# Performance work log

Measured on AMD Instinct MI355X. Metric: run time of the kernel, lower is better.

The kernel has to match this reference:

```python
import jax, jax.numpy as jnp
import numpy as np

N = 50000   # num_embs = num nodes
E = 800000  # num edges
D = 256     # feature dim
L = 4       # num layers
EPS = 1e-5


def setup_inputs() -> dict:
    key = jax.random.key(0)
    ks = jax.random.split(key, 8)
    scale = 1.0 / np.sqrt(D)
    return {
        "x": jax.random.normal(ks[0], (N, D), dtype=jnp.float32),  # ignored by forward
        "edge_index": jax.random.randint(ks[1], (2, E), 0, N, dtype=jnp.int32),
        "edge_weight": jax.random.uniform(ks[2], (E,), dtype=jnp.float32),
        "emb_weight": jax.random.normal(ks[3], (N, D), dtype=jnp.float32),
        "ln_w": jnp.ones((L, D), dtype=jnp.float32),
        "ln_b": jnp.zeros((L, D), dtype=jnp.float32),
        "conv_w": jax.random.normal(ks[4], (L, D, D), dtype=jnp.float32) * scale,
        "conv_b": jnp.zeros((L, D), dtype=jnp.float32),
        "post_w": jax.random.normal(ks[5], (D, D), dtype=jnp.float32) * scale,
        "post_b": jnp.zeros((D,), dtype=jnp.float32),
    }


def _layer_norm(h, w, b):
    mu = jnp.mean(h, axis=-1, keepdims=True)
    var = jnp.mean(jnp.square(h - mu), axis=-1, keepdims=True)
    return (h - mu) * jax.lax.rsqrt(var + EPS) * w + b


def reference(x, edge_index, edge_weight, emb_weight, ln_w, ln_b, conv_w, conv_b, post_w, post_b):
    # GCNConv semantics (PyG defaults): add self-loops (weight 1), symmetric norm.
    loop = jnp.arange(N, dtype=edge_index.dtype)
    src = jnp.concatenate([edge_index[0], loop])
    dst = jnp.concatenate([edge_index[1], loop])
    w = jnp.concatenate([edge_weight, jnp.ones((N,), edge_weight.dtype)])
    deg = jax.ops.segment_sum(w, dst, num_segments=N)
    dinv = jnp.where(deg > 0, jax.lax.rsqrt(jnp.maximum(deg, 1e-12)), 0.0)
    coef = (dinv[src] * w * dinv[dst])[:, None]  # [E+N, 1]

    h = emb_weight  # forward ignores x; cond_emb is None
    for i in range(L):
        z = _layer_norm(h, ln_w[i], ln_b[i])          # node LayerNorm
        zw = z @ conv_w[i]                             # linear transform
        agg = jax.ops.segment_sum(coef * zw[src], dst, num_segments=N)
        z = agg + conv_b[i]
        z = jax.nn.gelu(z, approximate=False)          # torch GELU is exact
        h = z + h                                      # residual (dropout=0)
    return h @ post_w + post_b
```

## Files before the change

kernel.cpp:

```cpp
#include <hip/hip_runtime.h>
#include <hip/hip_bf16.h>

#define N_NODES 50000
#define N_EDGES 800000
#define DIM     256
#define NLAYERS 4
#define EPS     1e-5f
#define SCAN_B  196
#define MASK40  ((1ULL << 40) - 1)
#define EPACK_CAP (N_EDGES + 15 * N_NODES + 32)
#define STRIDE  260

typedef __bf16 bf16x8 __attribute__((ext_vector_type(8)));
typedef float  f32x4  __attribute__((ext_vector_type(4)));
typedef float  f32x2  __attribute__((ext_vector_type(2)));
typedef unsigned short u16x8 __attribute__((ext_vector_type(8)));
typedef unsigned short u16x4 __attribute__((ext_vector_type(4)));
typedef int            i32x4 __attribute__((ext_vector_type(4)));
typedef unsigned int   u32x2 __attribute__((ext_vector_type(2)));

__device__ __forceinline__ unsigned short f2b(float f) {
    __hip_bfloat16 h = __float2bfloat16(f);
    return __builtin_bit_cast(unsigned short, h);
}
__device__ __forceinline__ float b2f(unsigned short u) {
    unsigned int v = ((unsigned int)u) << 16;
    return __builtin_bit_cast(float, v);
}
__device__ __forceinline__ float gelu_exact(float x) {
    return 0.5f * x * (1.0f + erff(x * 0.70710678118654752f));
}
__device__ __forceinline__ unsigned int pack_fp8x4(float a, float b, float c, float d) {
    int v = 0;
    v = __builtin_amdgcn_cvt_pk_fp8_f32(a, b, v, false);
    v = __builtin_amdgcn_cvt_pk_fp8_f32(c, d, v, true);
    return (unsigned int)v;
}

__global__ __launch_bounds__(256) void hist_kernel(const int* __restrict__ dst,
                                                   const float* __restrict__ w,
                                                   unsigned long long* __restrict__ cnt64,
                                                   int* __restrict__ rank) {
    int e = blockIdx.x * 256 + threadIdx.x;
    if (e >= N_EDGES) return;
    int d = dst[e];
    unsigned long long wfix = (unsigned long long)(w[e] * 4294967296.0f);
    unsigned long long old = atomicAdd(&cnt64[d], (1ULL << 40) | wfix);
    rank[e] = (int)(old >> 40);
}

__global__ __launch_bounds__(256) void scan_a_kernel(const unsigned long long* __restrict__ cnt64,
                                                     float* __restrict__ dinv,
                                                     int* __restrict__ bsum) {
    __shared__ int l[256];
    int i = blockIdx.x * 256 + threadIdx.x;
    int pc = 0;
    if (i < N_NODES) {
        unsigned long long v = cnt64[i];
        int cnt = (int)(v >> 40);
        float sw = (float)(v & MASK40) * 2.3283064365386963e-10f;
        dinv[i] = rsqrtf(1.0f + sw);
        pc = (cnt + 15) & ~15;
    }
    l[threadIdx.x] = pc;
    __syncthreads();
    for (int o = 128; o > 0; o >>= 1) {
        if (threadIdx.x < o) l[threadIdx.x] += l[threadIdx.x + o];
        __syncthreads();
    }
    if (threadIdx.x == 0) bsum[blockIdx.x] = l[0];
}

__global__ __launch_bounds__(256) void scan_b_kernel(const int* __restrict__ bsum,
                                                     int* __restrict__ boff,
                                                     int* __restrict__ rowptr) {
    __shared__ int l[256];
    int t = threadIdx.x;
    l[t] = (t < SCAN_B) ? bsum[t] : 0;
    __syncthreads();
    if (t == 0) {
        int run = 0;
        for (int j = 0; j < SCAN_B; ++j) { int v = l[j]; l[j] = run; run += v; }
        rowptr[N_NODES] = run;
    }
    __syncthreads();
    boff[t] = l[t];
}

__global__ __launch_bounds__(256) void scan_c_kernel(const unsigned long long* __restrict__ cnt64,
                                                     const int* __restrict__ boff,
                                                     int* __restrict__ rowptr) {
    __shared__ int l[256];
    int i = blockIdx.x * 256 + threadIdx.x;
    int pc = 0;
    if (i < N_NODES) {
        int cnt = (int)(cnt64[i] >> 40);
        pc = (cnt + 15) & ~15;
    }
    l[threadIdx.x] = pc;
    __syncthreads();
    if (threadIdx.x == 0) {
        int run = 0;
        for (int j = 0; j < 256; ++j) { int v = l[j]; l[j] = run; run += v; }
    }
    __syncthreads();
    if (i < N_NODES) rowptr[i] = boff[blockIdx.x] + l[threadIdx.x];
}

__global__ __launch_bounds__(256) void fill_kernel(const int* __restrict__ src,
                                                   const int* __restrict__ dst,
                                                   const float* __restrict__ w,
                                                   const float* __restrict__ dinv,
                                                   const int* __restrict__ rowptr,
                                                   const int* __restrict__ rank,
                                                   int2* __restrict__ epack) {
    int e = blockIdx.x * 256 + threadIdx.x;
    if (e >= N_EDGES) return;
    int s = src[e], d = dst[e];
    float c = dinv[s] * w[e] * dinv[d];
    int p = rowptr[d] + rank[e];
    epack[p] = make_int2(s << 8, __float_as_int(c));
}

__global__ __launch_bounds__(256) void convw_kernel(const float* __restrict__ conv_w,
                                                    const float* __restrict__ post_w,
                                                    unsigned short* __restrict__ Wt) {
    int idx = blockIdx.x * 256 + threadIdx.x;
    if (idx >= 5 * 65536) return;
    int m = idx >> 16;
    int r = idx & 65535;
    int n = r >> 8;
    int k = r & 255;
    float v = (m < 4) ? conv_w[m * 65536 + k * 256 + n] : post_w[k * 256 + n];
    Wt[idx] = f2b(v);
}

__global__ __launch_bounds__(256) void ln_cast_kernel(const float* __restrict__ H,
                                                      const float* __restrict__ lnw,
                                                      const float* __restrict__ lnb,
                                                      unsigned char* __restrict__ Z8,
                                                      unsigned short* __restrict__ Hbf) {
    int row = blockIdx.x * 4 + (threadIdx.x >> 6);
    int lane = threadIdx.x & 63;
    const float4 x = *(const float4*)(H + (size_t)row * DIM + lane * 4);
    float s = x.x + x.y + x.z + x.w;
    for (int o = 32; o > 0; o >>= 1) s += __shfl_xor(s, o);
    float mu = s * (1.0f / DIM);
    float d0 = x.x - mu, d1 = x.y - mu, d2 = x.z - mu, d3 = x.w - mu;
    float v = d0 * d0 + d1 * d1 + d2 * d2 + d3 * d3;
    for (int o = 32; o > 0; o >>= 1) v += __shfl_xor(v, o);
    float rs = rsqrtf(v * (1.0f / DIM) + EPS);
    const float4 ww = *(const float4*)(lnw + lane * 4);
    const float4 bb = *(const float4*)(lnb + lane * 4);
    float z0 = d0 * rs * ww.x + bb.x;
    float z1 = d1 * rs * ww.y + bb.y;
    float z2 = d2 * rs * ww.z + bb.z;
    float z3 = d3 * rs * ww.w + bb.w;
    *(unsigned int*)(Z8 + (size_t)row * DIM + lane * 4) = pack_fp8x4(z0, z1, z2, z3);
    ushort4 h4;
    h4.x = f2b(x.x); h4.y = f2b(x.y); h4.z = f2b(x.z); h4.w = f2b(x.w);
    *(ushort4*)(Hbf + (size_t)row * DIM + lane * 4) = h4;
}

__global__ __launch_bounds__(256) void agg_kernel(const unsigned char* __restrict__ Z8,
                                                  const int* __restrict__ rowptr,
                                                  const int2* __restrict__ epack,
                                                  const float* __restrict__ dinv,
                                                  unsigned short* __restrict__ AGG) {
    int node = blockIdx.x * 4 + (threadIdx.x >> 6);
    int lane = threadIdx.x & 63;
    int g = lane >> 5;
    int colB = (lane & 31) * 8;

    float di = dinv[node];
    float scg = (g == 0) ? di * di : 0.0f;
    const u32x2 zs = *(const u32x2*)(Z8 + (size_t)node * DIM + colB);
    f32x2 a0, a1, a2, a3;
    {
        f32x2 p0 = __builtin_amdgcn_cvt_pk_f32_fp8(zs[0], false);
        f32x2 p1 = __builtin_amdgcn_cvt_pk_f32_fp8(zs[0], true);
        f32x2 p2 = __builtin_amdgcn_cvt_pk_f32_fp8(zs[1], false);
        f32x2 p3 = __builtin_amdgcn_cvt_pk_f32_fp8(zs[1], true);
        a0 = scg * p0; a1 = scg * p1; a2 = scg * p2; a3 = scg * p3;
    }

    int e0 = rowptr[node], e1 = rowptr[node + 1];
    for (int e = e0; e < e1; e += 16) {
        const int2* pp = epack + e + 8 * g;
        const i32x4 q0 = *(const i32x4*)pp;
        const i32x4 q1 = *(const i32x4*)(pp + 2);
        const i32x4 q2 = *(const i32x4*)(pp + 4);
        const i32x4 q3 = *(const i32x4*)(pp + 6);
        const u32x2 v0 = *(const u32x2*)(Z8 + q0[0] + colB);
        const u32x2 v1 = *(const u32x2*)(Z8 + q0[2] + colB);
        const u32x2 v2 = *(const u32x2*)(Z8 + q1[0] + colB);
        const u32x2 v3 = *(const u32x2*)(Z8 + q1[2] + colB);
        const u32x2 v4 = *(const u32x2*)(Z8 + q2[0] + colB);
        const u32x2 v5 = *(const u32x2*)(Z8 + q2[2] + colB);
        const u32x2 v6 = *(const u32x2*)(Z8 + q3[0] + colB);
        const u32x2 v7 = *(const u32x2*)(Z8 + q3[2] + colB);
        float c0 = __int_as_float(q0[1]), c1 = __int_as_float(q0[3]);
        float c2 = __int_as_float(q1[1]), c3 = __int_as_float(q1[3]);
        float c4 = __int_as_float(q2[1]), c5 = __int_as_float(q2[3]);
        float c6 = __int_as_float(q3[1]), c7 = __int_as_float(q3[3]);
        #pragma unroll
        for (int h = 0; h < 8; ++h) {
            u32x2 vv; float cc;
            switch (h) {
                case 0: vv = v0; cc = c0; break;
                case 1: vv = v1; cc = c1; break;
                case 2: vv = v2; cc = c2; break;
                case 3: vv = v3; cc = c3; break;
                case 4: vv = v4; cc = c4; break;
                case 5: vv = v5; cc = c5; break;
                case 6: vv = v6; cc = c6; break;
                default: vv = v7; cc = c7; break;
            }
            f32x2 p0 = __builtin_amdgcn_cvt_pk_f32_fp8(vv[0], false);
            f32x2 p1 = __builtin_amdgcn_cvt_pk_f32_fp8(vv[0], true);
            f32x2 p2 = __builtin_amdgcn_cvt_pk_f32_fp8(vv[1], false);
            f32x2 p3 = __builtin_amdgcn_cvt_pk_f32_fp8(vv[1], true);
            a0 += cc * p0; a1 += cc * p1; a2 += cc * p2; a3 += cc * p3;
        }
    }
    float a[8] = {a0[0], a0[1], a1[0], a1[1], a2[0], a2[1], a3[0], a3[1]};
    #pragma unroll
    for (int j = 0; j < 8; ++j) a[j] += __shfl_xor(a[j], 32);

    if (g == 0) {
        u16x8 z;
        #pragma unroll
        for (int j = 0; j < 8; ++j) z[j] = f2b(a[j]);
        *(u16x8*)(AGG + (size_t)node * DIM + colB) = z;
    }
}

__global__ __launch_bounds__(256, 4) void gemm_fused_kernel(const unsigned short* __restrict__ A,
                                                            const unsigned short* __restrict__ Bt,
                                                            const float* __restrict__ bias,
                                                            unsigned short* __restrict__ Hbf,
                                                            const float* __restrict__ lnw,
                                                            const float* __restrict__ lnb,
                                                            unsigned char* __restrict__ Z8,
                                                            int doLN) {
    __shared__ unsigned short stile[32 * STRIDE];
    int tid = threadIdx.x;
    int wave = tid >> 6;
    int lane = tid & 63;
    int q = lane >> 4;
    int c16 = lane & 15;
    int mbase = blockIdx.x * 32;
    int cbase = wave * 64;

    const unsigned short* aptr[2];
    #pragma unroll
    for (int nt = 0; nt < 2; ++nt) {
        int row = mbase + nt * 16 + c16;
        if (row >= N_NODES) row = N_NODES - 1;
        aptr[nt] = A + (size_t)row * DIM + q * 8;
    }
    const unsigned short* wptr[4];
    #pragma unroll
    for (int ct = 0; ct < 4; ++ct)
        wptr[ct] = Bt + (size_t)(cbase + ct * 16 + c16) * DIM + q * 8;

    f32x4 acc[2][4] = {};
    bf16x8 nfc[2], wfc[4];
    #pragma unroll
    for (int nt = 0; nt < 2; ++nt)
        nfc[nt] = __builtin_bit_cast(bf16x8, *(const u16x8*)(aptr[nt]));
    #pragma unroll
    for (int ct = 0; ct < 4; ++ct)
        wfc[ct] = __builtin_bit_cast(bf16x8, *(const u16x8*)(wptr[ct]));

    #pragma unroll 1
    for (int k0 = 32; k0 < DIM; k0 += 32) {
        bf16x8 nfn[2], wfn[4];
        #pragma unroll
        for (int nt = 0; nt < 2; ++nt)
            nfn[nt] = __builtin_bit_cast(bf16x8, *(const u16x8*)(aptr[nt] + k0));
        #pragma unroll
        for (int ct = 0; ct < 4; ++ct)
            wfn[ct] = __builtin_bit_cast(bf16x8, *(const u16x8*)(wptr[ct] + k0));
        #pragma unroll
        for (int nt = 0; nt < 2; ++nt)
            #pragma unroll
            for (int ct = 0; ct < 4; ++ct)
                acc[nt][ct] = __builtin_amdgcn_mfma_f32_16x16x32_bf16(wfc[ct], nfc[nt], acc[nt][ct], 0, 0, 0);
        #pragma unroll
        for (int nt = 0; nt < 2; ++nt) nfc[nt] = nfn[nt];
        #pragma unroll
        for (int ct = 0; ct < 4; ++ct) wfc[ct] = wfn[ct];
    }
    #pragma unroll
    for (int nt = 0; nt < 2; ++nt)
        #pragma unroll
        for (int ct = 0; ct < 4; ++ct)
            acc[nt][ct] = __builtin_amdgcn_mfma_f32_16x16x32_bf16(wfc[ct], nfc[nt], acc[nt][ct], 0, 0, 0);

    #pragma unroll
    for (int nt = 0; nt < 2; ++nt) {
        int row = nt * 16 + c16;
        #pragma unroll
        for (int ct = 0; ct < 4; ++ct) {
            int col = cbase + ct * 16 + q * 4;
            u16x4 pk;
            pk[0] = f2b(acc[nt][ct][0]);
            pk[1] = f2b(acc[nt][ct][1]);
            pk[2] = f2b(acc[nt][ct][2]);
            pk[3] = f2b(acc[nt][ct][3]);
            *(u16x4*)&stile[row * STRIDE + col] = pk;
        }
    }
    __syncthreads();

    int r  = tid >> 3;
    int cb = (tid & 7) * 32;
    int node = mbase + r;
    if (node < N_NODES) {
        float h[32];
        float psum = 0.0f, psq = 0.0f;
        #pragma unroll
        for (int i = 0; i < 4; ++i) {
            const u16x8 sv = *(const u16x8*)&stile[r * STRIDE + cb + i * 8];
            const f32x4 b0 = *(const f32x4*)(bias + cb + i * 8);
            const f32x4 b1 = *(const f32x4*)(bias + cb + i * 8 + 4);
            const u16x8 hv = *(const u16x8*)(Hbf + (size_t)node * DIM + cb + i * 8);
            #pragma unroll
            for (int j = 0; j < 8; ++j) {
                float v = b2f(sv[j]) + (j < 4 ? b0[j] : b1[j - 4]);
                float hn = gelu_exact(v) + b2f(hv[j]);
                h[i * 8 + j] = hn;
                psum += hn;
                psq += hn * hn;
            }
        }
        #pragma unroll
        for (int i = 0; i < 4; ++i) {
            u16x8 hw;
            #pragma unroll
            for (int j = 0; j < 8; ++j) hw[j] = f2b(h[i * 8 + j]);
            *(u16x8*)(Hbf + (size_t)node * DIM + cb + i * 8) = hw;
        }
        if (doLN) {
            psum += __shfl_xor(psum, 1);
            psum += __shfl_xor(psum, 2);
            psum += __shfl_xor(psum, 4);
            psq  += __shfl_xor(psq, 1);
            psq  += __shfl_xor(psq, 2);
            psq  += __shfl_xor(psq, 4);
            float mu = psum * (1.0f / DIM);
            float var = fmaxf(psq * (1.0f / DIM) - mu * mu, 0.0f);
            float rs = rsqrtf(var + EPS);
            #pragma unroll
            for (int i2 = 0; i2 < 2; ++i2) {
                int c0 = cb + i2 * 16;
                unsigned int pk[4];
                #pragma unroll
                for (int k = 0; k < 4; ++k) {
                    const f32x4 ww = *(const f32x4*)(lnw + c0 + k * 4);
                    const f32x4 lb = *(const f32x4*)(lnb + c0 + k * 4);
                    int hb = i2 * 16 + k * 4;
                    float y0 = (h[hb + 0] - mu) * rs * ww[0] + lb[0];
                    float y1 = (h[hb + 1] - mu) * rs * ww[1] + lb[1];
                    float y2 = (h[hb + 2] - mu) * rs * ww[2] + lb[2];
                    float y3 = (h[hb + 3] - mu) * rs * ww[3] + lb[3];
                    pk[k] = pack_fp8x4(y0, y1, y2, y3);
                }
                uint4 st = make_uint4(pk[0], pk[1], pk[2], pk[3]);
                *(uint4*)(Z8 + (size_t)node * DIM + c0) = st;
            }
        }
    }
}

__global__ __launch_bounds__(256, 4) void gemm_out_kernel(const unsigned short* __restrict__ A,
                                                          const unsigned short* __restrict__ Bt,
                                                          float* __restrict__ C,
                                                          const float* __restrict__ bias) {
    int tid = threadIdx.x;
    int wave = tid >> 6;
    int lane = tid & 63;
    int q = lane >> 4;
    int c16 = lane & 15;
    int mbase = blockIdx.x * 32;
    int cbase = wave * 64;

    const unsigned short* aptr[2];
    #pragma unroll
    for (int nt = 0; nt < 2; ++nt) {
        int row = mbase + nt * 16 + c16;
        if (row >= N_NODES) row = N_NODES - 1;
        aptr[nt] = A + (size_t)row * DIM + q * 8;
    }
    const unsigned short* wptr[4];
    #pragma unroll
    for (int ct = 0; ct < 4; ++ct)
        wptr[ct] = Bt + (size_t)(cbase + ct * 16 + c16) * DIM + q * 8;

    f32x4 acc[2][4] = {};
    bf16x8 nfc[2], wfc[4];
    #pragma unroll
    for (int nt = 0; nt < 2; ++nt)
        nfc[nt] = __builtin_bit_cast(bf16x8, *(const u16x8*)(aptr[nt]));
    #pragma unroll
    for (int ct = 0; ct < 4; ++ct)
        wfc[ct] = __builtin_bit_cast(bf16x8, *(const u16x8*)(wptr[ct]));

    #pragma unroll 1
    for (int k0 = 32; k0 < DIM; k0 += 32) {
        bf16x8 nfn[2], wfn[4];
        #pragma unroll
        for (int nt = 0; nt < 2; ++nt)
            nfn[nt] = __builtin_bit_cast(bf16x8, *(const u16x8*)(aptr[nt] + k0));
        #pragma unroll
        for (int ct = 0; ct < 4; ++ct)
            wfn[ct] = __builtin_bit_cast(bf16x8, *(const u16x8*)(wptr[ct] + k0));
        #pragma unroll
        for (int nt = 0; nt < 2; ++nt)
            #pragma unroll
            for (int ct = 0; ct < 4; ++ct)
                acc[nt][ct] = __builtin_amdgcn_mfma_f32_16x16x32_bf16(nfc[nt], wfc[ct], acc[nt][ct], 0, 0, 0);
        #pragma unroll
        for (int nt = 0; nt < 2; ++nt) nfc[nt] = nfn[nt];
        #pragma unroll
        for (int ct = 0; ct < 4; ++ct) wfc[ct] = wfn[ct];
    }
    #pragma unroll
    for (int nt = 0; nt < 2; ++nt)
        #pragma unroll
        for (int ct = 0; ct < 4; ++ct)
            acc[nt][ct] = __builtin_amdgcn_mfma_f32_16x16x32_bf16(nfc[nt], wfc[ct], acc[nt][ct], 0, 0, 0);

    float bb[4];
    #pragma unroll
    for (int ct = 0; ct < 4; ++ct)
        bb[ct] = bias[cbase + ct * 16 + c16];
    #pragma unroll
    for (int nt = 0; nt < 2; ++nt) {
        #pragma unroll
        for (int j = 0; j < 4; ++j) {
            int node = mbase + nt * 16 + q * 4 + j;
            if (node >= N_NODES) continue;
            #pragma unroll
            for (int ct = 0; ct < 4; ++ct) {
                int chan = cbase + ct * 16 + c16;
                C[(size_t)node * DIM + chan] = acc[nt][ct][j] + bb[ct];
            }
        }
    }
}

extern "C" void kernel_launch(void* const* d_in, const int* in_sizes, int n_in,
                              void* d_out, int out_size, void* d_ws, size_t ws_size,
                              hipStream_t stream) {
    const int*   ei     = (const int*)d_in[1];
    const int*   src    = ei;
    const int*   dst    = ei + N_EDGES;
    const float* ew     = (const float*)d_in[2];
    const float* emb    = (const float*)d_in[3];
    const float* ln_w   = (const float*)d_in[4];
    const float* ln_b   = (const float*)d_in[5];
    const float* conv_w = (const float*)d_in[6];
    const float* conv_b = (const float*)d_in[7];
    const float* post_w = (const float*)d_in[8];
    const float* post_b = (const float*)d_in[9];
    float* out = (float*)d_out;

    char* w = (char*)d_ws;
    size_t off = 0;
    auto alloc = [&](size_t bytes) -> char* {
        char* p = w + off;
        off += (bytes + 255) & ~(size_t)255;
        return p;
    };
    unsigned long long* cnt64 = (unsigned long long*)alloc((size_t)N_NODES * 8);
    float* dinv   = (float*)alloc((size_t)N_NODES * 4);
    int*   rank   = (int*)alloc((size_t)N_EDGES * 4);
    int*   rowptr = (int*)alloc((size_t)(N_NODES + 1) * 4);
    int*   bsum   = (int*)alloc(256 * 4);
    int*   boff   = (int*)alloc(256 * 4);
    int2*  epack  = (int2*)alloc((size_t)EPACK_CAP * 8);
    unsigned short* Wt    = (unsigned short*)alloc((size_t)5 * 65536 * 2);
    unsigned short* AGG16 = (unsigned short*)alloc((size_t)N_NODES * DIM * 2);
    unsigned char*  Z8    = (unsigned char*)alloc((size_t)N_NODES * DIM);
    unsigned short* Hbf   = (unsigned short*)alloc((size_t)N_NODES * DIM * 2);

    hipMemsetAsync(cnt64, 0, (size_t)N_NODES * 8, stream);
    hipMemsetAsync(epack, 0, (size_t)EPACK_CAP * 8, stream);
    hist_kernel<<<N_EDGES / 256, 256, 0, stream>>>(dst, ew, cnt64, rank);
    scan_a_kernel<<<SCAN_B, 256, 0, stream>>>(cnt64, dinv, bsum);
    scan_b_kernel<<<1, 256, 0, stream>>>(bsum, boff, rowptr);
    scan_c_kernel<<<SCAN_B, 256, 0, stream>>>(cnt64, boff, rowptr);
    fill_kernel<<<N_EDGES / 256, 256, 0, stream>>>(src, dst, ew, dinv, rowptr, rank, epack);
    convw_kernel<<<(5 * 65536) / 256, 256, 0, stream>>>(conv_w, post_w, Wt);

    const int GEMM_GRID = (N_NODES + 31) / 32;
    ln_cast_kernel<<<N_NODES / 4, 256, 0, stream>>>(emb, ln_w, ln_b, Z8, Hbf);
    for (int l = 0; l < NLAYERS; ++l) {
        agg_kernel<<<N_NODES / 4, 256, 0, stream>>>(Z8, rowptr, epack, dinv, AGG16);
        int doLN = (l < NLAYERS - 1) ? 1 : 0;
        const float* nlw = doLN ? (ln_w + (l + 1) * DIM) : ln_w;
        const float* nlb = doLN ? (ln_b + (l + 1) * DIM) : ln_b;
        gemm_fused_kernel<<<GEMM_GRID, 256, 0, stream>>>(AGG16, Wt + (size_t)l * 65536,
                                                         conv_b + (size_t)l * DIM, Hbf,
                                                         nlw, nlb, Z8, doLN);
    }
    gemm_out_kernel<<<GEMM_GRID, 256, 0, stream>>>(Hbf, Wt + (size_t)4 * 65536, out, post_b);
}
```

Before: 653.3 us.

## Store aggregates and weights in K-sliced layout, fully unroll GEMM K-loop, approximate GELU

The weight transpose and the aggregation output now use a K-blocked layout of 32-wide column slabs, so each GEMM fragment load reads contiguous 64-byte rows within a slab. The GEMM K-loop is fully unrolled with direct indexed loads instead of manual double-buffered registers. Exact erf in GELU is replaced by an Abramowitz-Stegun polynomial with a fast exp. This trades some GELU accuracy and extra register pressure for better memory coalescing and cheaper math.

```diff
diff --git a/kernel.cpp b/kernel.cpp
--- a/kernel.cpp
+++ b/kernel.cpp
@@ -10,6 +10,7 @@
 #define MASK40  ((1ULL << 40) - 1)
 #define EPACK_CAP (N_EDGES + 15 * N_NODES + 32)
 #define STRIDE  260
+#define KSTRIDE (N_NODES * 32)
 
 typedef __bf16 bf16x8 __attribute__((ext_vector_type(8)));
 typedef float  f32x4  __attribute__((ext_vector_type(4)));
@@ -28,7 +29,13 @@
     return __builtin_bit_cast(float, v);
 }
 __device__ __forceinline__ float gelu_exact(float x) {
-    return 0.5f * x * (1.0f + erff(x * 0.70710678118654752f));
+    float ax = fabsf(x) * 0.70710678118654752f;
+    float t  = 1.0f / (1.0f + 0.3275911f * ax);
+    float p  = t * (0.254829592f + t * (-0.284496736f +
+               t * (1.421413741f + t * (-1.453152027f + t * 1.061405429f))));
+    float er = 1.0f - p * __expf(-ax * ax);
+    er = (x < 0.0f) ? -er : er;
+    return 0.5f * x * (1.0f + er);
 }
 __device__ __forceinline__ unsigned int pack_fp8x4(float a, float b, float c, float d) {
     int v = 0;
@@ -127,10 +134,12 @@
                                                     unsigned short* __restrict__ Wt) {
     int idx = blockIdx.x * 256 + threadIdx.x;
     if (idx >= 5 * 65536) return;
-    int m = idx >> 16;
-    int r = idx & 65535;
-    int n = r >> 8;
-    int k = r & 255;
+    int m  = idx >> 16;
+    int r  = idx & 65535;
+    int ks = r >> 13;
+    int n  = (r >> 5) & 255;
+    int ke = r & 31;
+    int k  = ks * 32 + ke;
     float v = (m < 4) ? conv_w[m * 65536 + k * 256 + n] : post_w[k * 256 + n];
     Wt[idx] = f2b(v);
 }
@@ -231,7 +240,9 @@
         u16x8 z;
         #pragma unroll
         for (int j = 0; j < 8; ++j) z[j] = f2b(a[j]);
-        *(u16x8*)(AGG + (size_t)node * DIM + colB) = z;
+        int ks  = colB >> 5;
+        int off = colB & 31;
+        *(u16x8*)(AGG + (size_t)ks * KSTRIDE + node * 32 + off) = z;
     }
 }
 
@@ -252,51 +263,34 @@
     int mbase = blockIdx.x * 32;
     int cbase = wave * 64;
 
-    const unsigned short* aptr[2];
+    int aoff[2];
     #pragma unroll
     for (int nt = 0; nt < 2; ++nt) {
         int row = mbase + nt * 16 + c16;
         if (row >= N_NODES) row = N_NODES - 1;
-        aptr[nt] = A + (size_t)row * DIM + q * 8;
-    }
-    const unsigned short* wptr[4];
+        aoff[nt] = row * 32 + q * 8;
+    }
+    int woff[4];
     #pragma unroll
     for (int ct = 0; ct < 4; ++ct)
-        wptr[ct] = Bt + (size_t)(cbase + ct * 16 + c16) * DIM + q * 8;
+        woff[ct] = (cbase + ct * 16 + c16) * 32 + q * 8;
 
     f32x4 acc[2][4] = {};
-    bf16x8 nfc[2], wfc[4];
-    #pragma unroll
-    for (int nt = 0; nt < 2; ++nt)
-        nfc[nt] = __builtin_bit_cast(bf16x8, *(const u16x8*)(aptr[nt]));
-    #pragma unroll
-    for (int ct = 0; ct < 4; ++ct)
-        wfc[ct] = __builtin_bit_cast(bf16x8, *(const u16x8*)(wptr[ct]));
-
-    #pragma unroll 1
-    for (int k0 = 32; k0 < DIM; k0 += 32) {
-        bf16x8 nfn[2], wfn[4];
+    #pragma unroll
+    for (int ks = 0; ks < 8; ++ks) {
+        bf16x8 nf[2], wf[4];
         #pragma unroll
         for (int nt = 0; nt < 2; ++nt)
-            nfn[nt] = __builtin_bit_cast(bf16x8, *(const u16x8*)(aptr[nt] + k0));
+            nf[nt] = __builtin_bit_cast(bf16x8, *(const u16x8*)(A + (size_t)ks * KSTRIDE + aoff[nt]));
         #pragma unroll
         for (int ct = 0; ct < 4; ++ct)
-            wfn[ct] = __builtin_bit_cast(bf16x8, *(const u16x8*)(wptr[ct] + k0));
+            wf[ct] = __builtin_bit_cast(bf16x8, *(const u16x8*)(Bt + ks * 8192 + woff[ct]));
         #pragma unroll
         for (int nt = 0; nt < 2; ++nt)
             #pragma unroll
             for (int ct = 0; ct < 4; ++ct)
-                acc[nt][ct] = __builtin_amdgcn_mfma_f32_16x16x32_bf16(wfc[ct], nfc[nt], acc[nt][ct], 0, 0, 0);
-        #pragma unroll
-        for (int nt = 0; nt < 2; ++nt) nfc[nt] = nfn[nt];
-        #pragma unroll
-        for (int ct = 0; ct < 4; ++ct) wfc[ct] = wfn[ct];
-    }
-    #pragma unroll
-    for (int nt = 0; nt < 2; ++nt)
-        #pragma unroll
-        for (int ct = 0; ct < 4; ++ct)
-            acc[nt][ct] = __builtin_amdgcn_mfma_f32_16x16x32_bf16(wfc[ct], nfc[nt], acc[nt][ct], 0, 0, 0);
+                acc[nt][ct] = __builtin_amdgcn_mfma_f32_16x16x32_bf16(wf[ct], nf[nt], acc[nt][ct], 0, 0, 0);
+    }
 
     #pragma unroll
     for (int nt = 0; nt < 2; ++nt) {
@@ -393,44 +387,27 @@
         if (row >= N_NODES) row = N_NODES - 1;
         aptr[nt] = A + (size_t)row * DIM + q * 8;
     }
-    const unsigned short* wptr[4];
+    int woff[4];
     #pragma unroll
     for (int ct = 0; ct < 4; ++ct)
-        wptr[ct] = Bt + (size_t)(cbase + ct * 16 + c16) * DIM + q * 8;
+        woff[ct] = (cbase + ct * 16 + c16) * 32 + q * 8;
 
     f32x4 acc[2][4] = {};
-    bf16x8 nfc[2], wfc[4];
-    #pragma unroll
-    for (int nt = 0; nt < 2; ++nt)
-        nfc[nt] = __builtin_bit_cast(bf16x8, *(const u16x8*)(aptr[nt]));
-    #pragma unroll
-    for (int ct = 0; ct < 4; ++ct)
-        wfc[ct] = __builtin_bit_cast(bf16x8, *(const u16x8*)(wptr[ct]));
-
-    #pragma unroll 1
-    for (int k0 = 32; k0 < DIM; k0 += 32) {
-        bf16x8 nfn[2], wfn[4];
+    #pragma unroll
+    for (int ks = 0; ks < 8; ++ks) {
+        bf16x8 nf[2], wf[4];
         #pragma unroll
         for (int nt = 0; nt < 2; ++nt)
-            nfn[nt] = __builtin_bit_cast(bf16x8, *(const u16x8*)(aptr[nt] + k0));
+            nf[nt] = __builtin_bit_cast(bf16x8, *(const u16x8*)(aptr[nt] + ks * 32));
         #pragma unroll
         for (int ct = 0; ct < 4; ++ct)
-            wfn[ct] = __builtin_bit_cast(bf16x8, *(const u16x8*)(wptr[ct] + k0));
+            wf[ct] = __builtin_bit_cast(bf16x8, *(const u16x8*)(Bt + ks * 8192 + woff[ct]));
         #pragma unroll
         for (int nt = 0; nt < 2; ++nt)
             #pragma unroll
             for (int ct = 0; ct < 4; ++ct)
-                acc[nt][ct] = __builtin_amdgcn_mfma_f32_16x16x32_bf16(nfc[nt], wfc[ct], acc[nt][ct], 0, 0, 0);
-        #pragma unroll
-        for (int nt = 0; nt < 2; ++nt) nfc[nt] = nfn[nt];
-        #pragma unroll
-        for (int ct = 0; ct < 4; ++ct) wfc[ct] = wfn[ct];
-    }
-    #pragma unroll
-    for (int nt = 0; nt < 2; ++nt)
-        #pragma unroll
-        for (int ct = 0; ct < 4; ++ct)
-            acc[nt][ct] = __builtin_amdgcn_mfma_f32_16x16x32_bf16(nfc[nt], wfc[ct], acc[nt][ct], 0, 0, 0);
+                acc[nt][ct] = __builtin_amdgcn_mfma_f32_16x16x32_bf16(nf[nt], wf[ct], acc[nt][ct], 0, 0, 0);
+    }
 
     float bb[4];
     #pragma unroll
```

Result: faster. 567.0 us (-13.2%).
